# Performance work log

Measured on AMD Instinct MI355X. Metric: run time of the kernel, lower is better.

Reference implementation:

```python
import jax, jax.numpy as jnp
import numpy as np

B = 16       # graphs per batch
N = 256      # nodes per graph (Hi-C submatrix bins)
NT = B * N   # total nodes
E = 131072   # total edges
DIN = 32     # input feature dim (HYPERPARAMETERS['input_shape'])
H1, H2 = 16, 32
HID = 32     # ContactCNN hidden dim
W7 = 7       # final conv width


def setup_inputs() -> dict:
    key = jax.random.key(0)
    ks = jax.random.split(key, 16)
    x = jax.random.normal(ks[0], (NT, DIN), dtype=jnp.float32)
    edge_index = jax.random.randint(ks[1], (2, E), 0, NT, dtype=jnp.int64)
    edge_attr = jax.random.uniform(ks[2], (E,), dtype=jnp.float32)
    batch_index = jnp.repeat(jnp.arange(B, dtype=jnp.int64), N)
    s = 0.1
    params = dict(
        W0=jax.random.normal(ks[3], (DIN, H1), dtype=jnp.float32) * s,
        b0=jnp.zeros((H1,), dtype=jnp.float32),
        W1=jax.random.normal(ks[4], (H1, H2), dtype=jnp.float32) * s,
        b1=jnp.zeros((H2,), dtype=jnp.float32),
        W2=jax.random.normal(ks[5], (H2, H2), dtype=jnp.float32) * s,
        b2=jnp.zeros((H2,), dtype=jnp.float32),
        Wc=jax.random.normal(ks[6], (HID, H2), dtype=jnp.float32) * s,  # 1x1 conv: [out=HID, in=H2]
        bc=jnp.zeros((HID,), dtype=jnp.float32),
        Wp=jax.random.normal(ks[7], (1, HID, W7, W7), dtype=jnp.float32) * s,  # OIHW
        bp=jnp.zeros((1,), dtype=jnp.float32),
    )
    return dict(x=x, edge_index=edge_index, edge_attr=edge_attr,
                batch_index=batch_index, **params)


def _gcn_norm(edge_index, edge_weight, n):
    # PyG gcn_norm with improved=True (self-loop fill value 2.0)
    src, dst = edge_index[0], edge_index[1]
    loop = jnp.arange(n, dtype=src.dtype)
    src_a = jnp.concatenate([src, loop])
    dst_a = jnp.concatenate([dst, loop])
    w_a = jnp.concatenate([edge_weight, jnp.full((n,), 2.0, dtype=edge_weight.dtype)])
    deg = jax.ops.segment_sum(w_a, dst_a, num_segments=n)
    deg_safe = jnp.where(deg > 0, deg, 1.0)
    dinv = jnp.where(deg > 0, jax.lax.rsqrt(deg_safe), 0.0)
    norm = dinv[src_a] * w_a * dinv[dst_a]
    return src_a, dst_a, norm


def _gcn_layer(h, W, b, src_a, dst_a, norm, n):
    h = h @ W                                  # [n, out]
    msg = norm[:, None] * h[src_a]             # gather + scale
    return jax.ops.segment_sum(msg, dst_a, num_segments=n) + b  # scatter-add


def reference(x, edge_index, edge_attr, batch_index,
              W0, b0, W1, b1, W2, b2, Wc, bc, Wp, bp):
    n = x.shape[0]
    src_a, dst_a, norm = _gcn_norm(edge_index, edge_attr, n)
    h = jax.nn.relu(_gcn_layer(x, W0, b0, src_a, dst_a, norm, n))
    h = jax.nn.relu(_gcn_layer(h, W1, b1, src_a, dst_a, norm, n))
    h = jax.nn.relu(_gcn_layer(h, W2, b2, src_a, dst_a, norm, n))
    z = h.reshape(B, N, -1)                    # process_graph_batch
    # ContactCNN: broadcast outer product -> 1x1 conv -> ReLU -> 7x7 conv -> sigmoid
    zm = jnp.einsum('bid,bjd->bdij', z, z)     # [B, D, N, N]
    c = jax.nn.relu(jnp.einsum('bdij,hd->bhij', zm, Wc) + bc[None, :, None, None])
    s = jax.lax.conv_general_dilated(
        c, Wp, window_strides=(1, 1), padding='SAME',
        dimension_numbers=('NCHW', 'OIHW', 'NCHW')) + bp[None, :, None, None]
    return jax.nn.sigmoid(s)                   # [B, 1, N, N]
```

## Files before the change

kernel.cpp:

```cpp
#include <hip/hip_runtime.h>
#include <hip/hip_bf16.h>
#include <hip/hip_fp16.h>

#define NT 4096
#define NE 131072

#define OFF_DEG  0
#define OFF_A    16384
#define OFF_G1T  33570816
#define OFF_G2T  33701888
#define OFF_G3T  33964032
#define OFF_H3   34226176
#define OFF_W2T  34488320

typedef __attribute__((ext_vector_type(8))) short bf16x8;
typedef __attribute__((ext_vector_type(4))) float f32x4;

__device__ inline unsigned int align16(unsigned int hi, unsigned int lo) {
#if __has_builtin(__builtin_amdgcn_alignbit)
    return __builtin_amdgcn_alignbit(hi, lo, 16);
#else
    return (lo >> 16) | (hi << 16);
#endif
}

__device__ inline unsigned short bfb(float x) {
    return __hip_bfloat16_raw(__float2bfloat16(x)).x;
}

__device__ inline void atomic_add_bf16(unsigned short* base, unsigned int idx, float v) {
    unsigned long long addr = (unsigned long long)(base + (idx & ~1u));
    unsigned int bits = ((unsigned int)bfb(v)) << ((idx & 1u) * 16);
    asm volatile("global_atomic_pk_add_bf16 %0, %1, off" :: "v"(addr), "v"(bits) : "memory");
}


__global__ __launch_bounds__(256) void k_zerodeg(const int* __restrict__ ei,
                                                 const float* __restrict__ ew,
                                                 float* __restrict__ deg,
                                                 unsigned short* __restrict__ A16) {
    int blk = blockIdx.x, tid = threadIdx.x;
    uint4 z4 = {0u, 0u, 0u, 0u};
    uint4* ap = (uint4*)(A16 + (size_t)blk * 16384);
    #pragma unroll
    for (int k = 0; k < 8; k++) ap[tid + k * 256] = z4;
    int gid = blk * 256 + tid;
    if (gid < NE) atomicAdd(&deg[ei[NE + gid]], ew[gid]);
}

__global__ void k_scatter(const int* __restrict__ ei, const float* __restrict__ ew,
                          const float* __restrict__ deg, unsigned short* __restrict__ A16,
                          const float* __restrict__ x, const float* __restrict__ W0,
                          unsigned short* __restrict__ G1T,
                          const float* __restrict__ Wp, unsigned int* __restrict__ w2) {
    int e = blockIdx.x * 256 + threadIdx.x;
    if (e < NE) {
        int s = ei[e], d = ei[NE + e];
        float v = rsqrtf(deg[s] + 2.f) * ew[e] * rsqrtf(deg[d] + 2.f);
        atomic_add_bf16(A16, (unsigned int)d * 4096u + (unsigned int)s, v);
    }
    if (e < NT) {
        atomic_add_bf16(A16, (unsigned int)e * 4097u, 2.f / (deg[e] + 2.f));
    }
    if (e < NT * 16) {
        int node = e & 4095, co = e >> 12;
        const float4* xr = (const float4*)(x + node * 32);
        float a = 0.f;
        #pragma unroll
        for (int r = 0; r < 8; r++) {
            float4 f = xr[r];
            a += f.x * W0[(r*4+0)*16 + co] + f.y * W0[(r*4+1)*16 + co]
               + f.z * W0[(r*4+2)*16 + co] + f.w * W0[(r*4+3)*16 + co];
        }
        G1T[co * 4096 + node] = bfb(a);
    }
    if (e >= NE - 1568) {
        int k = e - (NE - 1568);
        __half hh = __float2half(Wp[k]);
        __half2 h2 = __halves2half2(hh, hh);
        w2[k] = *(unsigned int*)&h2;
    }
}


template <int NIN, int NOUT, bool LAST>
__global__ __launch_bounds__(512) void k_gcn(const unsigned short* __restrict__ A16,
                                             const unsigned short* __restrict__ Gt,
                                             const float* __restrict__ bias,
                                             const float* __restrict__ W,
                                             unsigned short* __restrict__ Gout) {
    constexpr int T = NIN / 16;
    __shared__ float red[8][T][16][16];
    __shared__ unsigned short wtile[16 * 40];
    int mt = blockIdx.x;
    int tid = threadIdx.x;
    int w = tid >> 6, lane = tid & 63, m = lane & 15, q = lane >> 4;
    int kw = w * 512;

    const unsigned short* arow = A16 + (size_t)(mt * 16 + m) * 4096 + kw + q * 8;

    bf16x8 bA[16];
    #pragma unroll
    for (int s = 0; s < 16; s++) bA[s] = *(const bf16x8*)(arow + s * 32);

    f32x4 acc[T];
    #pragma unroll
    for (int t = 0; t < T; t++) acc[t] = (f32x4){0.f, 0.f, 0.f, 0.f};

    bf16x8 wfrag;
    if (!LAST && w < NOUT / 16) {
        #pragma unroll
        for (int j = 0; j < 8; j++) {
            int ci = q * 8 + j;
            wfrag[j] = (ci < NIN) ? (short)bfb(W[ci * NOUT + w * 16 + m]) : (short)0;
        }
    }

    const unsigned short* gbase = Gt + kw + q * 8 + (size_t)m * 4096;
    #pragma unroll
    for (int s = 0; s < 16; s++) {
        #pragma unroll
        for (int t = 0; t < T; t++) {
            bf16x8 af = *(const bf16x8*)(gbase + (size_t)t * 16 * 4096 + s * 32);
            acc[t] = __builtin_amdgcn_mfma_f32_16x16x32_bf16(af, bA[s], acc[t], 0, 0, 0);
        }
    }
    #pragma unroll
    for (int t = 0; t < T; t++)
        #pragma unroll
        for (int r = 0; r < 4; r++) red[w][t][q*4 + r][m] = acc[t][r];
    __syncthreads();

    if (tid < T * 256) {
        int dstp = tid & 15, cop = (tid >> 4) & 15, t = tid >> 8;
        float sum = 0.f;
        #pragma unroll
        for (int w8 = 0; w8 < 8; w8++) sum += red[w8][t][cop][dstp];
        int co = t * 16 + cop;
        float val = fmaxf(sum + bias[co], 0.f);
        if (LAST) Gout[(size_t)(mt * 16 + dstp) * 32 + co] = bfb(val);
        else      wtile[dstp * 40 + co] = bfb(val);
    }
    if (!LAST && NIN == 16 && tid >= 256 && tid < 512) {
        int idx = tid - 256;
        wtile[(idx & 15) * 40 + 16 + ((idx >> 4) & 15)] = 0;
    }
    __syncthreads();

    if (!LAST && w < NOUT / 16) {
        bf16x8 af = *(const bf16x8*)&wtile[m * 40 + q * 8];
        f32x4 o = (f32x4){0.f, 0.f, 0.f, 0.f};
        o = __builtin_amdgcn_mfma_f32_16x16x32_bf16(af, wfrag, o, 0, 0, 0);
        uint2 ov;
        ov.x = (unsigned int)bfb(o[0]) | ((unsigned int)bfb(o[1]) << 16);
        ov.y = (unsigned int)bfb(o[2]) | ((unsigned int)bfb(o[3]) << 16);
        *(uint2*)&Gout[(size_t)(w * 16 + m) * 4096 + mt * 16 + q * 4] = ov;
    }
}


__global__ __launch_bounds__(512, 4) void k_cc(const unsigned short* __restrict__ h3,
                                               const float* __restrict__ Wc,
                                               const float* __restrict__ bc,
                                               const unsigned int* __restrict__ w2,
                                               const float* __restrict__ bp,
                                               float* __restrict__ out) {
    __shared__ __align__(16) unsigned short pool[15680];
    __shared__ float wcs[32 * 36];

    int band = blockIdx.x, bb = blockIdx.y;
    int i0 = band * 8;
    int tid = threadIdx.x;
    int lane = tid & 63, w = tid >> 6;
    int m = lane & 15, q = lane >> 4;

    {
        int row = tid >> 1, half = tid & 1;
        const uint4* src = (const uint4*)(h3 + (size_t)(bb * 256 + row) * 32) + half * 2;
        uint4 v0 = src[0], v1 = src[1];
        uint4* dst = (uint4*)&pool[row * 40 + half * 16];
        dst[0] = v0; dst[1] = v1;
    }
    #pragma unroll
    for (int k = tid; k < 1024; k += 512) wcs[(k >> 5) * 36 + (k & 31)] = Wc[k];
    __syncthreads();

    bf16x8 bt;
    bool wok;
    {
        int r = i0 - 3 + m;
        wok = ((unsigned)r < 256u) && (m < 14);
        int rc = r < 0 ? 0 : (r > 255 ? 255 : r);
        bt = *(const bf16x8*)&pool[rc * 40 + q * 8];
    }
    float zaf[2][8];
    #pragma unroll
    for (int jt2 = 0; jt2 < 2; jt2++) {
        bf16x8 za = *(const bf16x8*)&pool[((w * 2 + jt2) * 16 + m) * 40 + q * 8];
        #pragma unroll
        for (int e = 0; e < 8; e++)
            zaf[jt2][e] = __uint_as_float(((unsigned int)(unsigned short)za[e]) << 16);
    }
    __syncthreads();

    for (int k = tid; k < 7840; k += 512) ((unsigned int*)pool)[k] = 0;
    __syncthreads();

    int gg = tid >> 7, idx = tid & 127;
    int tx = idx & 31, ty = idx >> 5;
    __half2 acc[2][4];
    __half2 zh = __float2half2_rn(0.f);
    #pragma unroll
    for (int o = 0; o < 2; o++)
        #pragma unroll
        for (int p = 0; p < 4; p++) acc[o][p] = zh;

    for (int it = 0; it < 8; it++) {
        #pragma unroll
        for (int g = 0; g < 4; g++) {
            int h = it * 4 + g;
            float wf[8];
            *(float4*)&wf[0] = *(const float4*)&wcs[h * 36 + q * 8];
            *(float4*)&wf[4] = *(const float4*)&wcs[h * 36 + q * 8 + 4];
            float bch = bc[h];
            #pragma unroll
            for (int jt2 = 0; jt2 < 2; jt2++) {
                bf16x8 afv;
                #pragma unroll
                for (int e = 0; e < 8; e++) afv[e] = (short)bfb(zaf[jt2][e] * wf[e]);
                int pos = 4 + (w * 2 + jt2) * 16 + q * 4;
                f32x4 d = (f32x4){0.f, 0.f, 0.f, 0.f};
                d = __builtin_amdgcn_mfma_f32_16x16x32_bf16(afv, bt, d, 0, 0, 0);
                if (wok) {
                    float v0 = fmaxf(d[0] + bch, 0.f);
                    float v1 = fmaxf(d[1] + bch, 0.f);
                    float v2 = fmaxf(d[2] + bch, 0.f);
                    float v3 = fmaxf(d[3] + bch, 0.f);
                    __half2 h0 = __floats2half2_rn(v0, v1);
                    __half2 h1 = __floats2half2_rn(v2, v3);
                    uint2 o2;
                    o2.x = *(unsigned int*)&h0;
                    o2.y = *(unsigned int*)&h1;
                    *(uint2*)&pool[g * 3920 + m * 280 + pos] = o2;
                }
            }
        }
        __syncthreads();

        {
            const unsigned short* C = pool + gg * 3920;
            const __half2* wrow = (const __half2*)w2 + (it * 4 + gg) * 49;
            #pragma unroll
            for (int dr = 0; dr < 8; dr++) {
                const uint4* p4 = (const uint4*)&C[(ty * 2 + dr) * 280 + tx * 8];
                uint4 ua = p4[0], ub = p4[1];
                unsigned int E[8] = {ua.x, ua.y, ua.z, ua.w, ub.x, ub.y, ub.z, ub.w};
                unsigned int O[7];
                #pragma unroll
                for (int k = 0; k < 7; k++) O[k] = align16(E[k + 1], E[k]);
                #pragma unroll
                for (int o = 0; o < 2; o++) {
                    if (dr - o < 0 || dr - o > 6) continue;
                    int di = dr - o;
                    #pragma unroll
                    for (int dj = 0; dj < 7; dj++) {
                        __half2 wv = wrow[di * 7 + dj];
                        #pragma unroll
                        for (int pr = 0; pr < 4; pr++) {
                            int s = 2 * pr + dj + 1;
                            unsigned int pv = (s & 1) ? O[s >> 1] : E[s >> 1];
                            acc[o][pr] = __hfma2(wv, *(__half2*)&pv, acc[o][pr]);
                        }
                    }
                }
            }
        }
        __syncthreads();
    }

    #pragma unroll
    for (int o = 0; o < 2; o++) {
        uint4 v;
        v.x = *(unsigned int*)&acc[o][0];
        v.y = *(unsigned int*)&acc[o][1];
        v.z = *(unsigned int*)&acc[o][2];
        v.w = *(unsigned int*)&acc[o][3];
        *(uint4*)&pool[gg * 2048 + (ty * 2 + o) * 256 + tx * 8] = v;
    }
    __syncthreads();

    {
        int base = tid * 4;
        float fs[4] = {0.f, 0.f, 0.f, 0.f};
        #pragma unroll
        for (int g = 0; g < 4; g++) {
            uint2 v = *(const uint2*)&pool[g * 2048 + base];
            float2 f0 = __half22float2(*(__half2*)&v.x);
            float2 f1 = __half22float2(*(__half2*)&v.y);
            fs[0] += f0.x; fs[1] += f0.y; fs[2] += f1.x; fs[3] += f1.y;
        }
        float bpv = bp[0];
        float4 r;
        r.x = 1.0f / (1.0f + __expf(-(fs[0] + bpv)));
        r.y = 1.0f / (1.0f + __expf(-(fs[1] + bpv)));
        r.z = 1.0f / (1.0f + __expf(-(fs[2] + bpv)));
        r.w = 1.0f / (1.0f + __expf(-(fs[3] + bpv)));
        int row = base >> 8, col = base & 255;
        *(float4*)&out[((size_t)(bb * 256) + i0 + row) * 256 + col] = r;
    }
}


extern "C" void kernel_launch(void* const* d_in, const int* in_sizes, int n_in,
                              void* d_out, int out_size, void* d_ws, size_t ws_size,
                              hipStream_t stream) {
    const float* x  = (const float*)d_in[0];
    const int*   ei = (const int*)d_in[1];
    const float* ew = (const float*)d_in[2];
    const float* W0 = (const float*)d_in[4];
    const float* b0 = (const float*)d_in[5];
    const float* W1 = (const float*)d_in[6];
    const float* b1 = (const float*)d_in[7];
    const float* W2 = (const float*)d_in[8];
    const float* b2 = (const float*)d_in[9];
    const float* Wc = (const float*)d_in[10];
    const float* bc = (const float*)d_in[11];
    const float* Wp = (const float*)d_in[12];
    const float* bp = (const float*)d_in[13];

    char* ws = (char*)d_ws;
    float*          deg  = (float*)(ws + OFF_DEG);
    unsigned short* A16  = (unsigned short*)(ws + OFF_A);
    unsigned short* G1T  = (unsigned short*)(ws + OFF_G1T);
    unsigned short* G2T  = (unsigned short*)(ws + OFF_G2T);
    unsigned short* G3T  = (unsigned short*)(ws + OFF_G3T);
    unsigned short* H3   = (unsigned short*)(ws + OFF_H3);
    unsigned int*   w2t  = (unsigned int*)(ws + OFF_W2T);

    (void)hipMemsetAsync(deg, 0, 16384, stream);

    k_zerodeg<<<1024, 256, 0, stream>>>(ei, ew, deg, A16);
    k_scatter<<<NE/256, 256, 0, stream>>>(ei, ew, deg, A16, x, W0, G1T, Wp, w2t);

    k_gcn<16, 32, false><<<256, 512, 0, stream>>>(A16, G1T, b0, W1, G2T);
    k_gcn<32, 32, false><<<256, 512, 0, stream>>>(A16, G2T, b1, W2, G3T);
    k_gcn<32, 32, true> <<<256, 512, 0, stream>>>(A16, G3T, b2, nullptr, H3);

    k_cc<<<dim3(32, 16), 512, 0, stream>>>(H3, Wc, bc, w2t, bp, (float*)d_out);
}
```

Baseline: 196.3 us.

## Split contact conv into half-width tiles and prefetch GCN operands into registers

Result: no change. 196.0 us (-0.1%).

```diff
diff --git a/kernel.cpp b/kernel.cpp
--- a/kernel.cpp
+++ b/kernel.cpp
@@ -98,10 +98,17 @@
     int kw = w * 512;
 
     const unsigned short* arow = A16 + (size_t)(mt * 16 + m) * 4096 + kw + q * 8;
+    const unsigned short* gbase = Gt + kw + q * 8 + (size_t)m * 4096;
 
     bf16x8 bA[16];
     #pragma unroll
     for (int s = 0; s < 16; s++) bA[s] = *(const bf16x8*)(arow + s * 32);
+    bf16x8 gf[16][T];
+    #pragma unroll
+    for (int s = 0; s < 16; s++)
+        #pragma unroll
+        for (int t = 0; t < T; t++)
+            gf[s][t] = *(const bf16x8*)(gbase + (size_t)t * 16 * 4096 + s * 32);
 
     f32x4 acc[T];
     #pragma unroll
@@ -116,15 +123,12 @@
         }
     }
 
-    const unsigned short* gbase = Gt + kw + q * 8 + (size_t)m * 4096;
-    #pragma unroll
-    for (int s = 0; s < 16; s++) {
-        #pragma unroll
-        for (int t = 0; t < T; t++) {
-            bf16x8 af = *(const bf16x8*)(gbase + (size_t)t * 16 * 4096 + s * 32);
-            acc[t] = __builtin_amdgcn_mfma_f32_16x16x32_bf16(af, bA[s], acc[t], 0, 0, 0);
-        }
-    }
+    #pragma unroll
+    for (int s = 0; s < 16; s++)
+        #pragma unroll
+        for (int t = 0; t < T; t++)
+            acc[t] = __builtin_amdgcn_mfma_f32_16x16x32_bf16(gf[s][t], bA[s], acc[t], 0, 0, 0);
+
     #pragma unroll
     for (int t = 0; t < T; t++)
         #pragma unroll
@@ -165,11 +169,11 @@
                                                const unsigned int* __restrict__ w2,
                                                const float* __restrict__ bp,
                                                float* __restrict__ out) {
-    __shared__ __align__(16) unsigned short pool[15680];
+    __shared__ __align__(16) unsigned short pool[10240];
     __shared__ float wcs[32 * 36];
-
-    int band = blockIdx.x, bb = blockIdx.y;
-    int i0 = band * 8;
+    __shared__ __align__(16) unsigned short pt[4][1024];
+
+    int j0 = blockIdx.x * 128, i0 = blockIdx.y * 8, bb = blockIdx.z;
     int tid = threadIdx.x;
     int lane = tid & 63, w = tid >> 6;
     int m = lane & 15, q = lane >> 4;
@@ -185,35 +189,44 @@
     for (int k = tid; k < 1024; k += 512) wcs[(k >> 5) * 36 + (k & 31)] = Wc[k];
     __syncthreads();
 
-    bf16x8 bt;
+    float btf[8];
     bool wok;
     {
         int r = i0 - 3 + m;
         wok = ((unsigned)r < 256u) && (m < 14);
         int rc = r < 0 ? 0 : (r > 255 ? 255 : r);
-        bt = *(const bf16x8*)&pool[rc * 40 + q * 8];
-    }
-    float zaf[2][8];
-    #pragma unroll
-    for (int jt2 = 0; jt2 < 2; jt2++) {
-        bf16x8 za = *(const bf16x8*)&pool[((w * 2 + jt2) * 16 + m) * 40 + q * 8];
+        bf16x8 bt = *(const bf16x8*)&pool[rc * 40 + q * 8];
         #pragma unroll
         for (int e = 0; e < 8; e++)
-            zaf[jt2][e] = __uint_as_float(((unsigned int)(unsigned short)za[e]) << 16);
-    }
-    __syncthreads();
-
-    for (int k = tid; k < 7840; k += 512) ((unsigned int*)pool)[k] = 0;
+            btf[e] = __uint_as_float(((unsigned int)(unsigned short)bt[e]) << 16);
+    }
+    bf16x8 zfr;
+    #pragma unroll
+    for (int e = 0; e < 8; e++) zfr[e] = 0;
+    bf16x8 afm, afx;
+    {
+        int jr = j0 - 3 + w * 16 + m;
+        bool ok = (unsigned)jr < 256u;
+        int jc = jr < 0 ? 0 : (jr > 255 ? 255 : jr);
+        afm = *(const bf16x8*)&pool[jc * 40 + q * 8];
+        if (!ok) afm = zfr;
+        int jr8 = j0 + 125 + m;
+        bool ok8 = (unsigned)jr8 < 256u;
+        int jc8 = jr8 > 255 ? 255 : jr8;
+        afx = *(const bf16x8*)&pool[jc8 * 40 + q * 8];
+        if (!ok8) afx = zfr;
+    }
+    __syncthreads();
+
+    for (int k = tid; k < 4032; k += 512) ((unsigned int*)pool)[k] = 0;
     __syncthreads();
 
     int gg = tid >> 7, idx = tid & 127;
-    int tx = idx & 31, ty = idx >> 5;
-    __half2 acc[2][4];
+    int tx = idx & 15, ty = idx >> 4;
+    __half2 acc[4];
     __half2 zh = __float2half2_rn(0.f);
     #pragma unroll
-    for (int o = 0; o < 2; o++)
-        #pragma unroll
-        for (int p = 0; p < 4; p++) acc[o][p] = zh;
+    for (int p = 0; p < 4; p++) acc[p] = zh;
 
     for (int it = 0; it < 8; it++) {
         #pragma unroll
@@ -223,54 +236,62 @@
             *(float4*)&wf[0] = *(const float4*)&wcs[h * 36 + q * 8];
             *(float4*)&wf[4] = *(const float4*)&wcs[h * 36 + q * 8 + 4];
             float bch = bc[h];
+            unsigned int bu[4];
             #pragma unroll
-            for (int jt2 = 0; jt2 < 2; jt2++) {
-                bf16x8 afv;
-                #pragma unroll
-                for (int e = 0; e < 8; e++) afv[e] = (short)bfb(zaf[jt2][e] * wf[e]);
-                int pos = 4 + (w * 2 + jt2) * 16 + q * 4;
+            for (int k = 0; k < 4; k++) {
+                float m0 = btf[2*k]   * wf[2*k];
+                float m1 = btf[2*k+1] * wf[2*k+1];
+                bu[k] = __builtin_amdgcn_perm(__float_as_uint(m1), __float_as_uint(m0),
+                                              0x07060302u);
+            }
+            bf16x8 btv;
+            *(uint4*)&btv = make_uint4(bu[0], bu[1], bu[2], bu[3]);
+            {
                 f32x4 d = (f32x4){0.f, 0.f, 0.f, 0.f};
-                d = __builtin_amdgcn_mfma_f32_16x16x32_bf16(afv, bt, d, 0, 0, 0);
+                d = __builtin_amdgcn_mfma_f32_16x16x32_bf16(afm, btv, d, 0, 0, 0);
                 if (wok) {
-                    float v0 = fmaxf(d[0] + bch, 0.f);
-                    float v1 = fmaxf(d[1] + bch, 0.f);
-                    float v2 = fmaxf(d[2] + bch, 0.f);
-                    float v3 = fmaxf(d[3] + bch, 0.f);
-                    __half2 h0 = __floats2half2_rn(v0, v1);
-                    __half2 h1 = __floats2half2_rn(v2, v3);
+                    __half2 h0 = __floats2half2_rn(fmaxf(d[0] + bch, 0.f), fmaxf(d[1] + bch, 0.f));
+                    __half2 h1 = __floats2half2_rn(fmaxf(d[2] + bch, 0.f), fmaxf(d[3] + bch, 0.f));
                     uint2 o2;
                     o2.x = *(unsigned int*)&h0;
                     o2.y = *(unsigned int*)&h1;
-                    *(uint2*)&pool[g * 3920 + m * 280 + pos] = o2;
+                    *(uint2*)&pool[g * 2016 + m * 144 + w * 16 + q * 4] = o2;
                 }
             }
+            if (w == 0) {
+                f32x4 d = (f32x4){0.f, 0.f, 0.f, 0.f};
+                d = __builtin_amdgcn_mfma_f32_16x16x32_bf16(afx, btv, d, 0, 0, 0);
+                if (wok) {
+                    __half2 h0 = __floats2half2_rn(fmaxf(d[0] + bch, 0.f), fmaxf(d[1] + bch, 0.f));
+                    __half2 h1 = __floats2half2_rn(fmaxf(d[2] + bch, 0.f), fmaxf(d[3] + bch, 0.f));
+                    uint2 o2;
+                    o2.x = *(unsigned int*)&h0;
+                    o2.y = *(unsigned int*)&h1;
+                    *(uint2*)&pool[g * 2016 + m * 144 + 128 + q * 4] = o2;
+                }
+            }
         }
         __syncthreads();
 
         {
-            const unsigned short* C = pool + gg * 3920;
+            const unsigned short* C = pool + gg * 2016;
             const __half2* wrow = (const __half2*)w2 + (it * 4 + gg) * 49;
             #pragma unroll
-            for (int dr = 0; dr < 8; dr++) {
-                const uint4* p4 = (const uint4*)&C[(ty * 2 + dr) * 280 + tx * 8];
+            for (int dr = 0; dr < 7; dr++) {
+                const uint4* p4 = (const uint4*)&C[(ty + dr) * 144 + tx * 8];
                 uint4 ua = p4[0], ub = p4[1];
                 unsigned int E[8] = {ua.x, ua.y, ua.z, ua.w, ub.x, ub.y, ub.z, ub.w};
-                unsigned int O[7];
+                unsigned int O[6];
                 #pragma unroll
-                for (int k = 0; k < 7; k++) O[k] = align16(E[k + 1], E[k]);
+                for (int k = 0; k < 6; k++) O[k] = align16(E[k + 1], E[k]);
                 #pragma unroll
-                for (int o = 0; o < 2; o++) {
-                    if (dr - o < 0 || dr - o > 6) continue;
-                    int di = dr - o;
+                for (int dj = 0; dj < 7; dj++) {
+                    __half2 wv = wrow[dr * 7 + dj];
                     #pragma unroll
-                    for (int dj = 0; dj < 7; dj++) {
-                        __half2 wv = wrow[di * 7 + dj];
-                        #pragma unroll
-                        for (int pr = 0; pr < 4; pr++) {
-                            int s = 2 * pr + dj + 1;
-                            unsigned int pv = (s & 1) ? O[s >> 1] : E[s >> 1];
-                            acc[o][pr] = __hfma2(wv, *(__half2*)&pv, acc[o][pr]);
-                        }
+                    for (int pr = 0; pr < 4; pr++) {
+                        int s = 2 * pr + dj;
+                        unsigned int pv = (s & 1) ? O[s >> 1] : E[s >> 1];
+                        acc[pr] = __hfma2(wv, *(__half2*)&pv, acc[pr]);
                     }
                 }
             }
@@ -278,35 +299,30 @@
         __syncthreads();
     }
 
-    #pragma unroll
-    for (int o = 0; o < 2; o++) {
+    {
         uint4 v;
-        v.x = *(unsigned int*)&acc[o][0];
-        v.y = *(unsigned int*)&acc[o][1];
-        v.z = *(unsigned int*)&acc[o][2];
-        v.w = *(unsigned int*)&acc[o][3];
-        *(uint4*)&pool[gg * 2048 + (ty * 2 + o) * 256 + tx * 8] = v;
-    }
-    __syncthreads();
-
-    {
-        int base = tid * 4;
-        float fs[4] = {0.f, 0.f, 0.f, 0.f};
+        v.x = *(unsigned int*)&acc[0];
+        v.y = *(unsigned int*)&acc[1];
+        v.z = *(unsigned int*)&acc[2];
+        v.w = *(unsigned int*)&acc[3];
+        *(uint4*)&pt[gg][idx * 8] = v;
+    }
+    __syncthreads();
+
+    {
+        float fs0 = 0.f, fs1 = 0.f;
         #pragma unroll
         for (int g = 0; g < 4; g++) {
-            uint2 v = *(const uint2*)&pool[g * 2048 + base];
-            float2 f0 = __half22float2(*(__half2*)&v.x);
-            float2 f1 = __half22float2(*(__half2*)&v.y);
-            fs[0] += f0.x; fs[1] += f0.y; fs[2] += f1.x; fs[3] += f1.y;
+            unsigned int u = ((unsigned int*)pt)[g * 512 + tid];
+            float2 f = __half22float2(*(__half2*)&u);
+            fs0 += f.x; fs1 += f.y;
         }
         float bpv = bp[0];
-        float4 r;
-        r.x = 1.0f / (1.0f + __expf(-(fs[0] + bpv)));
-        r.y = 1.0f / (1.0f + __expf(-(fs[1] + bpv)));
-        r.z = 1.0f / (1.0f + __expf(-(fs[2] + bpv)));
-        r.w = 1.0f / (1.0f + __expf(-(fs[3] + bpv)));
-        int row = base >> 8, col = base & 255;
-        *(float4*)&out[((size_t)(bb * 256) + i0 + row) * 256 + col] = r;
+        float2 r;
+        r.x = 1.0f / (1.0f + __expf(-(fs0 + bpv)));
+        r.y = 1.0f / (1.0f + __expf(-(fs1 + bpv)));
+        int row = tid >> 6, col = (tid * 2) & 127;
+        *(float2*)&out[((size_t)(bb * 256) + i0 + row) * 256 + j0 + col] = r;
     }
 }
 
@@ -346,5 +362,5 @@
     k_gcn<32, 32, false><<<256, 512, 0, stream>>>(A16, G2T, b1, W2, G3T);
     k_gcn<32, 32, true> <<<256, 512, 0, stream>>>(A16, G3T, b2, nullptr, H3);
 
-    k_cc<<<dim3(32, 16), 512, 0, stream>>>(H3, Wc, bc, w2t, bp, (float*)d_out);
-}
+    k_cc<<<dim3(2, 32, 16), 512, 0, stream>>>(H3, Wc, bc, w2t, bp, (float*)d_out);
+}
```
